# Kernel optimization log

Measured on AMD Instinct MI355X. Metric: run time of the kernel, lower is better.

The kernel has to match this reference:

```python
import jax, jax.numpy as jnp
import numpy as np

H, K, D, M = 16, 64, 1024, 4096
S, B = 2048, 4
EPS = 1e-5


def _ln(x, g, b):
    mu = jnp.mean(x, axis=-1, keepdims=True)
    var = jnp.var(x, axis=-1, keepdims=True)
    return (x - mu) / jnp.sqrt(var + EPS) * g + b


def setup_inputs() -> dict:
    key = jax.random.key(0)
    ks = jax.random.split(key, 8)
    std = 0.02
    x = jax.random.normal(ks[0], (S, B, D), jnp.float32)
    mask = jnp.zeros((S, S), jnp.float32)  # additive attention mask, broadcasts over (H*B, S, S)
    wq = jax.random.normal(ks[1], (H * K, D), jnp.float32) * std
    wk = jax.random.normal(ks[2], (H * K, D), jnp.float32) * std
    wv = jax.random.normal(ks[3], (H * K, D), jnp.float32) * std
    wc = jax.random.normal(ks[4], (D, H * K), jnp.float32) * std
    w1_w = jax.random.normal(ks[5], (M, D), jnp.float32) * std
    w1_b = jnp.zeros((M,), jnp.float32)
    w2_w = jax.random.normal(ks[6], (D, M), jnp.float32) * std
    w2_b = jnp.zeros((D,), jnp.float32)
    ln1_g = jnp.ones((D,), jnp.float32)
    ln1_b = jnp.zeros((D,), jnp.float32)
    ln2_g = jnp.ones((D,), jnp.float32)
    ln2_b = jnp.zeros((D,), jnp.float32)
    return dict(x=x, mask=mask, wq=wq, wk=wk, wv=wv, wc=wc, w1_w=w1_w, w1_b=w1_b,
                w2_w=w2_w, w2_b=w2_b, ln1_g=ln1_g, ln1_b=ln1_b, ln2_g=ln2_g, ln2_b=ln2_b)


def reference(x, mask, wq, wk, wv, wc, w1_w, w1_b, w2_w, w2_b, ln1_g, ln1_b, ln2_g, ln2_b):
    s, b, _ = x.shape
    q = (x @ wq.T).reshape(s, b, H, K)
    k = (x @ wk.T).reshape(s, b, H, K)
    v = (x @ wv.T).reshape(s, b, H, K)
    # scores: (B, H, S, S); mask (S, S) broadcasts over batch and heads as in torch
    scores = jnp.einsum('sbhk,tbhk->bhst', q, k) / jnp.sqrt(jnp.float32(K)) + mask
    alpha = jax.nn.softmax(scores, axis=-1)
    av = jnp.einsum('bhst,tbhk->sbhk', alpha, v).reshape(s, b, H * K)
    u = _ln(av @ wc.T + x, ln1_g, ln1_b)
    z = jax.nn.relu(u @ w1_w.T + w1_b) @ w2_w.T + w2_b
    return _ln(z + u, ln2_g, ln2_b)
```

## Files before the change

### kernel.cpp

```cpp
#include <hip/hip_runtime.h>
#include <math.h>

#define H_  16
#define K_  64
#define D_  1024
#define M_  4096
#define S_  2048
#define B_  4
#define N_  8192
#define HK_ 1024

typedef __attribute__((ext_vector_type(8))) short bfrag;
typedef __attribute__((ext_vector_type(4))) float f4;

typedef __attribute__((address_space(1))) const void g_void;
typedef __attribute__((address_space(3))) void s_void;

__device__ __forceinline__ float bf2f(unsigned short u){
  union { unsigned int i; float f; } x; x.i = ((unsigned int)u) << 16; return x.f;
}
__device__ __forceinline__ unsigned short f2bf(float f){
  unsigned int u = __float_as_uint(f);
  return (unsigned short)((u + 0x7fffu + ((u >> 16) & 1u)) >> 16);
}
__device__ __forceinline__ unsigned int pack2(float a, float b){
  return (unsigned int)f2bf(a) | ((unsigned int)f2bf(b) << 16);
}
__device__ __forceinline__ void gload16(const void* g, void* l){
  __builtin_amdgcn_global_load_lds((g_void*)g, (s_void*)l, 16, 0, 0);
}

__global__ __launch_bounds__(256) void castk(const float* __restrict__ in,
                                             unsigned short* __restrict__ out){
  int i = (blockIdx.x * 256 + threadIdx.x) * 4;
  float4 v = *(const float4*)(in + i);
  *(uint2*)(out + i) = make_uint2(pack2(v.x, v.y), pack2(v.z, v.w));
}

template<int EPI>
__global__ __launch_bounds__(256) void mgemm(
    const unsigned short* __restrict__ A, const unsigned short* __restrict__ W,
    const float* __restrict__ bias, const void* __restrict__ res,
    unsigned short* __restrict__ C, int Kdim, int Ncols)
{
  __shared__ unsigned short sA[4096];
  __shared__ unsigned short sB[4096];
  const int tid  = threadIdx.x;
  const int wave = tid >> 6, ln = tid & 63;
  const int lr   = ln & 15, quad = ln >> 4;
  const int m0   = blockIdx.y * 128, n0 = blockIdx.x * 128;
  const int wr   = (wave >> 1) * 64, wc = (wave & 1) * 64;
  const int segr = ln >> 2, segc = (ln & 3) * 8;
  const int sg   = wave * 2;

  const unsigned short* A0 = A + (size_t)(m0 + sg*16      + segr) * Kdim + segc;
  const unsigned short* A1 = A + (size_t)(m0 + sg*16 + 16 + segr) * Kdim + segc;
  const unsigned short* W0 = W + (size_t)(n0 + sg*16      + segr) * Kdim + segc;
  const unsigned short* W1 = W + (size_t)(n0 + sg*16 + 16 + segr) * Kdim + segc;

  const f4 zero = {0.f, 0.f, 0.f, 0.f};
  f4 acc[4][4];
  #pragma unroll
  for (int i=0;i<4;i++)
    #pragma unroll
    for (int j=0;j<4;j++) acc[i][j] = zero;

  for (int k0 = 0; k0 < Kdim; k0 += 32){
    gload16(A0 + k0, &sA[sg*512]);
    gload16(A1 + k0, &sA[sg*512 + 512]);
    gload16(W0 + k0, &sB[sg*512]);
    gload16(W1 + k0, &sB[sg*512 + 512]);
    __syncthreads();
    bfrag af[4], bf[4];
    #pragma unroll
    for (int i=0;i<4;i++) af[i] = *(const bfrag*)&sA[(wr + i*16 + lr)*32 + quad*8];
    #pragma unroll
    for (int j=0;j<4;j++) bf[j] = *(const bfrag*)&sB[(wc + j*16 + lr)*32 + quad*8];
    #pragma unroll
    for (int i=0;i<4;i++)
      #pragma unroll
      for (int j=0;j<4;j++)
        acc[i][j] = __builtin_amdgcn_mfma_f32_16x16x32_bf16(af[i], bf[j], acc[i][j], 0, 0, 0);
    __syncthreads();
  }

  #pragma unroll
  for (int i=0;i<4;i++){
    #pragma unroll
    for (int j=0;j<4;j++){
      #pragma unroll
      for (int r=0;r<4;r++){
        const int m = m0 + wr + i*16 + quad*4 + r;
        const int n = n0 + wc + j*16 + lr;
        float t = acc[i][j][r];
        if (EPI == 0){
          const int s = m >> 2, b = m & 3, h = n >> 6, kk = n & 63;
          C[(((size_t)(b*16 + h)) * S_ + s) * 64 + kk] = f2bf(t);
        } else {
          const size_t off = (size_t)m * Ncols + n;
          if (EPI == 1) t += ((const float*)res)[off];
          if (EPI == 2) t = fmaxf(t + bias[n], 0.f);
          if (EPI == 3) t += bias[n] + bf2f(((const unsigned short*)res)[off]);
          C[off] = f2bf(t);
        }
      }
    }
  }
}

__global__ __launch_bounds__(256) void vtrans(const unsigned short* __restrict__ v,
                                              unsigned short* __restrict__ vT){
  const int tid = threadIdx.x;
  const int wave = tid >> 6, ln = tid & 63;
  const int bh = blockIdx.y;
  const int s  = blockIdx.x * 64 + ln;
  const int d0 = wave * 16;
  unsigned short tmp[16];
  const unsigned short* src = v + ((size_t)bh * S_ + s) * 64 + d0;
  *(uint4*)&tmp[0] = ((const uint4*)src)[0];
  *(uint4*)&tmp[8] = ((const uint4*)src)[1];
  unsigned short* dst = vT + (size_t)bh * 64 * S_ + s;
  #pragma unroll
  for (int e = 0; e < 16; e++)
    dst[(size_t)(d0 + e) * S_] = tmp[e];
}

__global__ __launch_bounds__(256) void fattn(
    const unsigned short* __restrict__ qg, const unsigned short* __restrict__ kg,
    const unsigned short* __restrict__ vT, const float* __restrict__ mask,
    unsigned short* __restrict__ av)
{
  __shared__ unsigned short Ks[4096];
  __shared__ unsigned short VTs[4096];
  __shared__ unsigned short Ps[4*32*72];
  const int tid  = threadIdx.x;
  const int wave = tid >> 6, ln = tid & 63;
  const int lr   = ln & 15, quad = ln >> 4;
  const int bh   = blockIdx.y;
  const int b    = bh >> 4, h = bh & 15;
  const int s0   = blockIdx.x * 128;
  const size_t base  = (size_t)bh * S_ * 64;
  const size_t tbase = (size_t)bh * 64 * S_;
  const int qw = s0 + wave*32;

  bfrag aq[2][2];
  #pragma unroll
  for (int qb=0;qb<2;qb++)
    #pragma unroll
    for (int hh=0;hh<2;hh++)
      aq[qb][hh] = *(const bfrag*)(qg + base + (size_t)(qw + qb*16 + lr)*64 + hh*32 + quad*8);

  const f4 zero = {0.f, 0.f, 0.f, 0.f};
  f4 acc[2][4];
  #pragma unroll
  for (int qb=0;qb<2;qb++)
    #pragma unroll
    for (int nb=0;nb<4;nb++) acc[qb][nb] = zero;
  float lsum[2][4];
  #pragma unroll
  for (int qb=0;qb<2;qb++)
    #pragma unroll
    for (int r=0;r<4;r++) lsum[qb][r] = 0.f;

  const int strow = wave*16 + (ln >> 3);
  const int scol  = (ln & 7) * 8;
  unsigned short* const ksd0 = &Ks[(wave*16)*64];
  unsigned short* const ksd1 = &Ks[(wave*16 + 8)*64];
  unsigned short* const vtd0 = &VTs[(wave*16)*64];
  unsigned short* const vtd1 = &VTs[(wave*16 + 8)*64];

  unsigned short* const psw = &Ps[wave*2304];

  for (int t0 = 0; t0 < S_; t0 += 64){
    gload16(kg + base  + (size_t)(t0 + strow    )*64 + scol, ksd0);
    gload16(kg + base  + (size_t)(t0 + strow + 8)*64 + scol, ksd1);
    gload16(vT + tbase + (size_t)(strow    )*S_ + t0 + scol, vtd0);
    gload16(vT + tbase + (size_t)(strow + 8)*S_ + t0 + scol, vtd1);
    __syncthreads();

    bfrag kf[4][2];
    #pragma unroll
    for (int tb=0;tb<4;tb++)
      #pragma unroll
      for (int hh=0;hh<2;hh++)
        kf[tb][hh] = *(const bfrag*)&Ks[(tb*16 + lr)*64 + hh*32 + quad*8];

    #pragma unroll
    for (int qb=0;qb<2;qb++){
      f4 sc[4];
      #pragma unroll
      for (int tb=0;tb<4;tb++){
        f4 t = zero;
        t = __builtin_amdgcn_mfma_f32_16x16x32_bf16(aq[qb][0], kf[tb][0], t, 0, 0, 0);
        t = __builtin_amdgcn_mfma_f32_16x16x32_bf16(aq[qb][1], kf[tb][1], t, 0, 0, 0);
        sc[tb] = t;
      }
      #pragma unroll
      for (int tb=0;tb<4;tb++)
        #pragma unroll
        for (int r=0;r<4;r++){
          const int qrow = qw + qb*16 + quad*4 + r;
          float p = __expf(sc[tb][r]*0.125f + mask[(size_t)qrow*S_ + t0 + tb*16 + lr]);
          lsum[qb][r] += p;
          psw[(qb*16 + quad*4 + r)*72 + tb*16 + lr] = f2bf(p);
        }
    }

    bfrag vf[4][2];
    #pragma unroll
    for (int nb=0;nb<4;nb++)
      #pragma unroll
      for (int hh=0;hh<2;hh++)
        vf[nb][hh] = *(const bfrag*)&VTs[(nb*16 + lr)*64 + hh*32 + quad*8];
    #pragma unroll
    for (int qb=0;qb<2;qb++){
      bfrag ap0 = *(const bfrag*)&psw[(qb*16 + lr)*72 + quad*8];
      bfrag ap1 = *(const bfrag*)&psw[(qb*16 + lr)*72 + 32 + quad*8];
      #pragma unroll
      for (int nb=0;nb<4;nb++){
        acc[qb][nb] = __builtin_amdgcn_mfma_f32_16x16x32_bf16(ap0, vf[nb][0], acc[qb][nb], 0, 0, 0);
        acc[qb][nb] = __builtin_amdgcn_mfma_f32_16x16x32_bf16(ap1, vf[nb][1], acc[qb][nb], 0, 0, 0);
      }
    }
    __syncthreads();
  }

  #pragma unroll
  for (int qb=0;qb<2;qb++)
    #pragma unroll
    for (int r=0;r<4;r++){
      float l = lsum[qb][r];
      l += __shfl_xor(l, 1);
      l += __shfl_xor(l, 2);
      l += __shfl_xor(l, 4);
      l += __shfl_xor(l, 8);
      const float inv = 1.f / l;
      const int qrow = qw + qb*16 + quad*4 + r;
      #pragma unroll
      for (int nb=0;nb<4;nb++)
        av[((size_t)qrow * B_ + b) * HK_ + h*64 + nb*16 + lr] = f2bf(acc[qb][nb][r] * inv);
    }
}

template<int OUTF32>
__global__ __launch_bounds__(256) void lnk(
    const unsigned short* __restrict__ pre, const float* __restrict__ g,
    const float* __restrict__ be, void* __restrict__ out)
{
  __shared__ float red[256];
  const int row = blockIdx.x;
  const int tid = threadIdx.x;
  const unsigned short* p = pre + (size_t)row * D_;
  uint2 raw = *(const uint2*)(p + tid*4);
  float x[4] = { bf2f(raw.x & 0xffffu), bf2f(raw.x >> 16),
                 bf2f(raw.y & 0xffffu), bf2f(raw.y >> 16) };
  red[tid] = x[0] + x[1] + x[2] + x[3];
  __syncthreads();
  for (int q = 128; q > 0; q >>= 1){
    if (tid < q) red[tid] += red[tid + q];
    __syncthreads();
  }
  const float mu = red[0] * (1.f / (float)D_);
  __syncthreads();
  float d0 = x[0]-mu, d1 = x[1]-mu, d2 = x[2]-mu, d3 = x[3]-mu;
  red[tid] = d0*d0 + d1*d1 + d2*d2 + d3*d3;
  __syncthreads();
  for (int q = 128; q > 0; q >>= 1){
    if (tid < q) red[tid] += red[tid + q];
    __syncthreads();
  }
  const float rstd = rsqrtf(red[0] * (1.f / (float)D_) + 1e-5f);
  const int c = tid * 4;
  #pragma unroll
  for (int j=0;j<4;j++){
    float y = (x[j] - mu) * rstd * g[c + j] + be[c + j];
    if (OUTF32) ((float*)out)[(size_t)row * D_ + c + j] = y;
    else ((unsigned short*)out)[(size_t)row * D_ + c + j] = f2bf(y);
  }
}

extern "C" void kernel_launch(void* const* d_in, const int* in_sizes, int n_in,
                              void* d_out, int out_size, void* d_ws, size_t ws_size,
                              hipStream_t stream) {
  const float* x    = (const float*)d_in[0];
  const float* mask = (const float*)d_in[1];
  const float* wq   = (const float*)d_in[2];
  const float* wk   = (const float*)d_in[3];
  const float* wv   = (const float*)d_in[4];
  const float* wc   = (const float*)d_in[5];
  const float* w1w  = (const float*)d_in[6];
  const float* w1b  = (const float*)d_in[7];
  const float* w2w  = (const float*)d_in[8];
  const float* w2b  = (const float*)d_in[9];
  const float* g1   = (const float*)d_in[10];
  const float* b1   = (const float*)d_in[11];
  const float* g2   = (const float*)d_in[12];
  const float* b2   = (const float*)d_in[13];

  unsigned short* ws = (unsigned short*)d_ws;
  unsigned short* xb   = ws + 0;
  unsigned short* wqb  = ws + 8388608;
  unsigned short* wkb  = ws + 9437184;
  unsigned short* wvb  = ws + 10485760;
  unsigned short* wcb  = ws + 11534336;
  unsigned short* q    = ws + 12582912;
  unsigned short* k    = ws + 20971520;
  unsigned short* v    = ws + 29360128;
  unsigned short* w1wb = ws + 37748736;
  unsigned short* w2wb = ws + 41943040;
  unsigned short* u    = ws + 46137344;
  unsigned short* z    = ws + 54525952;
  unsigned short* vT   = z;
  unsigned short* avb  = ws + 0;
  unsigned short* t1   = ws + 12582912;
  unsigned short* h1   = ws + 0;

  castk<<<8192, 256, 0, stream>>>(x,   xb);
  castk<<<1024, 256, 0, stream>>>(wq,  wqb);
  castk<<<1024, 256, 0, stream>>>(wk,  wkb);
  castk<<<1024, 256, 0, stream>>>(wv,  wvb);
  castk<<<1024, 256, 0, stream>>>(wc,  wcb);
  castk<<<4096, 256, 0, stream>>>(w1w, w1wb);
  castk<<<4096, 256, 0, stream>>>(w2w, w2wb);

  mgemm<0><<<dim3(8, 64), 256, 0, stream>>>(xb, wqb, nullptr, nullptr, q, D_, HK_);
  mgemm<0><<<dim3(8, 64), 256, 0, stream>>>(xb, wkb, nullptr, nullptr, k, D_, HK_);
  mgemm<0><<<dim3(8, 64), 256, 0, stream>>>(xb, wvb, nullptr, nullptr, v, D_, HK_);

  vtrans<<<dim3(S_/64, 64), 256, 0, stream>>>(v, vT);
  fattn<<<dim3(S_/128, B_*H_), 256, 0, stream>>>(q, k, vT, mask, avb);

  mgemm<1><<<dim3(8, 64), 256, 0, stream>>>(avb, wcb, nullptr, x, t1, HK_, D_);
  lnk<0><<<dim3(N_), 256, 0, stream>>>(t1, g1, b1, u);

  mgemm<2><<<dim3(32, 64), 256, 0, stream>>>(u, w1wb, w1b, nullptr, h1, D_, M_);

  mgemm<3><<<dim3(8, 64), 256, 0, stream>>>(h1, w2wb, w2b, u, z, M_, D_);
  lnk<1><<<dim3(N_), 256, 0, stream>>>(z, g2, b2, d_out);
}
```

Measured before the change: 685.1 us.

## Double-buffer flash-attention K/V tiles with swizzled LDS and exp2 softmax

The attention kernel now double-buffers the K and V^T tiles in LDS, issuing the next tile's async global-to-LDS loads before computing on the current one. This removes one barrier per iteration and hides load latency. It also XOR-swizzles the LDS layout to cut bank conflicts, preloads the mask values into registers, and switches to exp2 with a mask pre-scaled by log2(e) in a new small kernel. It adds packed bf16 conversion and s_setprio hints around the MFMA sections, at the cost of more LDS and registers.

```diff
diff --git a/kernel.cpp b/kernel.cpp
--- a/kernel.cpp
+++ b/kernel.cpp
@@ -35,6 +35,15 @@
   int i = (blockIdx.x * 256 + threadIdx.x) * 4;
   float4 v = *(const float4*)(in + i);
   *(uint2*)(out + i) = make_uint2(pack2(v.x, v.y), pack2(v.z, v.w));
+}
+
+__global__ __launch_bounds__(256) void mscale(const float* __restrict__ in,
+                                              float* __restrict__ out){
+  int i = (blockIdx.x * 256 + threadIdx.x) * 4;
+  float4 v = *(const float4*)(in + i);
+  const float c = 1.44269504f;
+  v.x *= c; v.y *= c; v.z *= c; v.w *= c;
+  *(float4*)(out + i) = v;
 }
 
 template<int EPI>
@@ -127,11 +136,11 @@
 
 __global__ __launch_bounds__(256) void fattn(
     const unsigned short* __restrict__ qg, const unsigned short* __restrict__ kg,
-    const unsigned short* __restrict__ vT, const float* __restrict__ mask,
+    const unsigned short* __restrict__ vT, const float* __restrict__ mb,
     unsigned short* __restrict__ av)
 {
-  __shared__ unsigned short Ks[4096];
-  __shared__ unsigned short VTs[4096];
+  __shared__ unsigned short Ks[2][4096];
+  __shared__ unsigned short VTs[2][4096];
   __shared__ unsigned short Ps[4*32*72];
   const int tid  = threadIdx.x;
   const int wave = tid >> 6, ln = tid & 63;
@@ -163,31 +172,65 @@
     for (int r=0;r<4;r++) lsum[qb][r] = 0.f;
 
   const int strow = wave*16 + (ln >> 3);
-  const int scol  = (ln & 7) * 8;
-  unsigned short* const ksd0 = &Ks[(wave*16)*64];
-  unsigned short* const ksd1 = &Ks[(wave*16 + 8)*64];
-  unsigned short* const vtd0 = &VTs[(wave*16)*64];
-  unsigned short* const vtd1 = &VTs[(wave*16 + 8)*64];
+  const int scz   = ((ln & 7) ^ (ln >> 3)) * 8;
+  const int rxor  = lr & 7;
 
   unsigned short* const psw = &Ps[wave*2304];
 
+  const float* mrow[2][4];
+  #pragma unroll
+  for (int qb=0;qb<2;qb++)
+    #pragma unroll
+    for (int r=0;r<4;r++)
+      mrow[qb][r] = mb + (size_t)(qw + qb*16 + quad*4 + r) * S_ + lr;
+
+  auto stage = [&](int bufn, int t0n){
+    unsigned short* kd = &Ks[bufn][(wave*16)*64];
+    unsigned short* vd = &VTs[bufn][(wave*16)*64];
+    gload16(kg + base  + (size_t)(t0n + strow    )*64 + scz, kd);
+    gload16(kg + base  + (size_t)(t0n + strow + 8)*64 + scz, kd + 512);
+    gload16(vT + tbase + (size_t)(strow    )*S_ + t0n + scz, vd);
+    gload16(vT + tbase + (size_t)(strow + 8)*S_ + t0n + scz, vd + 512);
+  };
+
+  stage(0, 0);
+  int cur = 0;
+
   for (int t0 = 0; t0 < S_; t0 += 64){
-    gload16(kg + base  + (size_t)(t0 + strow    )*64 + scol, ksd0);
-    gload16(kg + base  + (size_t)(t0 + strow + 8)*64 + scol, ksd1);
-    gload16(vT + tbase + (size_t)(strow    )*S_ + t0 + scol, vtd0);
-    gload16(vT + tbase + (size_t)(strow + 8)*S_ + t0 + scol, vtd1);
-    __syncthreads();
+    __syncthreads();
+
+    float mreg[2][4][4];
+    #pragma unroll
+    for (int qb=0;qb<2;qb++)
+      #pragma unroll
+      for (int r=0;r<4;r++)
+        #pragma unroll
+        for (int tb=0;tb<4;tb++)
+          mreg[qb][r][tb] = mrow[qb][r][t0 + tb*16];
+
+    if (t0 + 64 < S_) stage(cur ^ 1, t0 + 64);
+
+    const unsigned short* Kc = Ks[cur];
+    const unsigned short* Vc = VTs[cur];
 
     bfrag kf[4][2];
     #pragma unroll
     for (int tb=0;tb<4;tb++)
       #pragma unroll
       for (int hh=0;hh<2;hh++)
-        kf[tb][hh] = *(const bfrag*)&Ks[(tb*16 + lr)*64 + hh*32 + quad*8];
+        kf[tb][hh] = *(const bfrag*)&Kc[(tb*16 + lr)*64 + (((hh*4 + quad) ^ rxor))*8];
+
+    bfrag vf[4][2];
+    #pragma unroll
+    for (int nb=0;nb<4;nb++)
+      #pragma unroll
+      for (int hh=0;hh<2;hh++)
+        vf[nb][hh] = *(const bfrag*)&Vc[(nb*16 + lr)*64 + (((hh*4 + quad) ^ rxor))*8];
 
     #pragma unroll
     for (int qb=0;qb<2;qb++){
       f4 sc[4];
+      __builtin_amdgcn_s_setprio(1);
       #pragma unroll
       for (int tb=0;tb<4;tb++){
         f4 t = zero;
@@ -195,23 +238,27 @@
         t = __builtin_amdgcn_mfma_f32_16x16x32_bf16(aq[qb][1], kf[tb][1], t, 0, 0, 0);
         sc[tb] = t;
       }
-      #pragma unroll
-      for (int tb=0;tb<4;tb++)
-        #pragma unroll
-        for (int r=0;r<4;r++){
-          const int qrow = qw + qb*16 + quad*4 + r;
-          float p = __expf(sc[tb][r]*0.125f + mask[(size_t)qrow*S_ + t0 + tb*16 + lr]);
-          lsum[qb][r] += p;
-          psw[(qb*16 + quad*4 + r)*72 + tb*16 + lr] = f2bf(p);
-        }
+      __builtin_amdgcn_s_setprio(0);
+      #pragma unroll
+      for (int tb=0;tb<4;tb++){
+        float p0 = __builtin_amdgcn_exp2f(fmaf(sc[tb][0], 0.18033688f, mreg[qb][0][tb]));
+        float p1 = __builtin_amdgcn_exp2f(fmaf(sc[tb][1], 0.18033688f, mreg[qb][1][tb]));
+        float p2 = __builtin_amdgcn_exp2f(fmaf(sc[tb][2], 0.18033688f, mreg[qb][2][tb]));
+        float p3 = __builtin_amdgcn_exp2f(fmaf(sc[tb][3], 0.18033688f, mreg[qb][3][tb]));
+        lsum[qb][0] += p0; lsum[qb][1] += p1;
+        lsum[qb][2] += p2; lsum[qb][3] += p3;
+        unsigned int pkA, pkB;
+        asm("v_cvt_pk_bf16_f32 %0, %1, %2" : "=v"(pkA) : "v"(p0), "v"(p1));
+        asm("v_cvt_pk_bf16_f32 %0, %1, %2" : "=v"(pkB) : "v"(p2), "v"(p3));
+        unsigned short* pp = &psw[(qb*16 + quad*4)*72 + tb*16 + lr];
+        pp[0]   = (unsigned short)pkA;
+        pp[72]  = (unsigned short)(pkA >> 16);
+        pp[144] = (unsigned short)pkB;
+        pp[216] = (unsigned short)(pkB >> 16);
+      }
     }
 
-    bfrag vf[4][2];
-    #pragma unroll
-    for (int nb=0;nb<4;nb++)
-      #pragma unroll
-      for (int hh=0;hh<2;hh++)
-        vf[nb][hh] = *(const bfrag*)&VTs[(nb*16 + lr)*64 + hh*32 + quad*8];
+    __builtin_amdgcn_s_setprio(1);
     #pragma unroll
     for (int qb=0;qb<2;qb++){
       bfrag ap0 = *(const bfrag*)&psw[(qb*16 + lr)*72 + quad*8];
@@ -222,7 +269,8 @@
         acc[qb][nb] = __builtin_amdgcn_mfma_f32_16x16x32_bf16(ap1, vf[nb][1], acc[qb][nb], 0, 0, 0);
       }
     }
-    __syncthreads();
+    __builtin_amdgcn_s_setprio(0);
+    cur ^= 1;
   }
 
   #pragma unroll
@@ -314,6 +362,7 @@
   unsigned short* avb  = ws + 0;
   unsigned short* t1   = ws + 12582912;
   unsigned short* h1   = ws + 0;
+  float*          mb   = (float*)(ws + 46137344);
 
   castk<<<8192, 256, 0, stream>>>(x,   xb);
   castk<<<1024, 256, 0, stream>>>(wq,  wqb);
@@ -322,13 +371,14 @@
   castk<<<1024, 256, 0, stream>>>(wc,  wcb);
   castk<<<4096, 256, 0, stream>>>(w1w, w1wb);
   castk<<<4096, 256, 0, stream>>>(w2w, w2wb);
+  mscale<<<4096, 256, 0, stream>>>(mask, mb);
 
   mgemm<0><<<dim3(8, 64), 256, 0, stream>>>(xb, wqb, nullptr, nullptr, q, D_, HK_);
   mgemm<0><<<dim3(8, 64), 256, 0, stream>>>(xb, wkb, nullptr, nullptr, k, D_, HK_);
   mgemm<0><<<dim3(8, 64), 256, 0, stream>>>(xb, wvb, nullptr, nullptr, v, D_, HK_);
 
   vtrans<<<dim3(S_/64, 64), 256, 0, stream>>>(v, vT);
-  fattn<<<dim3(S_/128, B_*H_), 256, 0, stream>>>(q, k, vT, mask, avb);
+  fattn<<<dim3(S_/128, B_*H_), 256, 0, stream>>>(q, k, vT, mb, avb);
 
   mgemm<1><<<dim3(8, 64), 256, 0, stream>>>(avb, wcb, nullptr, x, t1, HK_, D_);
   lnk<0><<<dim3(N_), 256, 0, stream>>>(t1, g1, b1, u);
```

Measured after the change: 650.6 us. -5.0%, faster.
